# Kernel tuning notes

Hardware: AMD Instinct MI355X
Metric: run time of the kernel (lower is better)

Reference implementation:

```python
import jax, jax.numpy as jnp
import numpy as np

B, T, X, H = 8192, 2048, 1, 4

def setup_inputs() -> dict:
    key = jax.random.key(0)
    ks = jax.random.split(key, 8)
    return {
        "x": jax.random.normal(ks[0], (B, T, X), dtype=jnp.float32),
        "y": (jax.random.uniform(ks[1], (B, T)) < 0.5).astype(jnp.float32),  # binary correctness labels
        "Wxh": jax.random.normal(ks[2], (X, H), dtype=jnp.float32) * 0.5,
        "Whh": jax.random.normal(ks[3], (H, H), dtype=jnp.float32) * 0.5,
        "bh": jax.random.normal(ks[4], (H,), dtype=jnp.float32) * 0.5,
        "Wy": jax.random.normal(ks[5], (H, 4), dtype=jnp.float32) * 0.5,
        "by": jax.random.normal(ks[6], (4,), dtype=jnp.float32) * 0.5,
        "prior": jnp.float32(0.0),
    }

def _bkt_forward(x, y, Wxh, Whh, bh, Wy, by, prior):
    # x: [B,T,X], y: [B,T]. Sequential BKT scan over time with batch vectorized.
    b = x.shape[0]
    h0 = jnp.zeros((b, Wy.shape[0]), dtype=x.dtype)
    lat0 = jnp.full((b,), prior, dtype=x.dtype)

    def step(carry, xt):
        h, latent = carry
        p = jax.nn.sigmoid(h @ Wy + by)          # [B,4] -> (learn l, forget f, guess g, slip s)
        l, f, g, s = p[:, 0], p[:, 1], p[:, 2], p[:, 3]
        correct = latent * (1 - s) + (1 - latent) * g
        k_t1 = latent * (1 - s) / correct
        k_t0 = latent * s / (latent * s + (1 - latent) * (1 - g))
        m_t = k_t1 * correct + k_t0 * (1 - correct)
        new_latent = m_t * (1 - f) + (1 - m_t) * l
        h_new = jax.nn.sigmoid(xt @ Wxh + h @ Whh + bh)  # [B,H]
        return (h_new, new_latent), (correct, new_latent)

    xs = jnp.swapaxes(x, 0, 1)                   # [T,B,X]
    _, (corrects, latents) = jax.lax.scan(step, (h0, lat0), xs)
    corrects = jnp.swapaxes(corrects, 0, 1)      # [B,T]
    latents = jnp.swapaxes(latents, 0, 1)        # [B,T]
    eps = jnp.float32(1e-7)
    c = jnp.clip(corrects, eps, 1 - eps)
    loss = -jnp.mean(y * jnp.log(c) + (1 - y) * jnp.log1p(-c))
    return corrects, latents, loss

def reference(x, y, Wxh, Whh, bh, Wy, by, prior):
    return _bkt_forward(x, y, Wxh, Whh, bh, Wy, by, prior)
```

## Files before the change

### kernel.cpp

```cpp
#include <hip/hip_runtime.h>

#define BB 8192
#define TT 2048
#define CLW 16
#define WU  8

typedef __fp16 f16x2 __attribute__((ext_vector_type(2)));

__device__ __forceinline__ float sig2(float z) {
    return __builtin_amdgcn_rcpf(1.f + __builtin_amdgcn_exp2f(z));
}
__device__ __forceinline__ float sgpr(float v) {
    return __builtin_bit_cast(float, __builtin_amdgcn_readfirstlane(__builtin_bit_cast(int, v)));
}
__device__ __forceinline__ void ld16(float* d, const float* p) {
    *(float4*)(d)      = *(const float4*)(p);
    *(float4*)(d + 4)  = *(const float4*)(p + 4);
    *(float4*)(d + 8)  = *(const float4*)(p + 8);
    *(float4*)(d + 12) = *(const float4*)(p + 12);
}

__global__ __launch_bounds__(256, 4) void bkt_fused(
    const float* __restrict__ x, const float* __restrict__ y,
    const float* __restrict__ Wxh, const float* __restrict__ Whh,
    const float* __restrict__ bh, const float* __restrict__ Wy,
    const float* __restrict__ by, const float* __restrict__ prior,
    float* __restrict__ corrects, float* __restrict__ latents,
    float* __restrict__ partials)
{
    __shared__ float lds[4 * 32 * 33];
    __shared__ float2 hand[2];
    const int tid  = blockIdx.x * 256 + threadIdx.x;
    const int lane = threadIdx.x & 63;
    const int wv   = threadIdx.x >> 6;
    const int half = wv & 1;
    const int rib  = wv >> 1;
    const int row  = blockIdx.x * 2 + rib;
    float* r0 = &lds[wv * 1056];
    const int wbase = (lane >> 1) * 33 + (lane & 1) * 16;
    const float NL2E = -1.44269504088896340736f;

    const float wh00=sgpr(Whh[0]*NL2E),  wh01=sgpr(Whh[1]*NL2E),
                wh02=sgpr(Whh[2]*NL2E),  wh03=sgpr(Whh[3]*NL2E),
                wh10=sgpr(Whh[4]*NL2E),  wh11=sgpr(Whh[5]*NL2E),
                wh12=sgpr(Whh[6]*NL2E),  wh13=sgpr(Whh[7]*NL2E),
                wh20=sgpr(Whh[8]*NL2E),  wh21=sgpr(Whh[9]*NL2E),
                wh22=sgpr(Whh[10]*NL2E), wh23=sgpr(Whh[11]*NL2E),
                wh30=sgpr(Whh[12]*NL2E), wh31=sgpr(Whh[13]*NL2E),
                wh32=sgpr(Whh[14]*NL2E), wh33=sgpr(Whh[15]*NL2E);
    const float wx0=sgpr(Wxh[0]*NL2E), wx1=sgpr(Wxh[1]*NL2E),
                wx2=sgpr(Wxh[2]*NL2E), wx3=sgpr(Wxh[3]*NL2E);
    const float bh0=sgpr(bh[0]*NL2E), bh1=sgpr(bh[1]*NL2E),
                bh2=sgpr(bh[2]*NL2E), bh3=sgpr(bh[3]*NL2E);
    const float wy00=sgpr(Wy[0]*NL2E),  wy01=sgpr(Wy[1]*NL2E),
                wy02=sgpr(Wy[2]*NL2E),  wy03=sgpr(Wy[3]*NL2E),
                wy10=sgpr(Wy[4]*NL2E),  wy11=sgpr(Wy[5]*NL2E),
                wy12=sgpr(Wy[6]*NL2E),  wy13=sgpr(Wy[7]*NL2E),
                wy20=sgpr(Wy[8]*NL2E),  wy21=sgpr(Wy[9]*NL2E),
                wy22=sgpr(Wy[10]*NL2E), wy23=sgpr(Wy[11]*NL2E),
                wy30=sgpr(Wy[12]*NL2E), wy31=sgpr(Wy[13]*NL2E),
                wy32=sgpr(Wy[14]*NL2E), wy33=sgpr(Wy[15]*NL2E);
    const float by0=sgpr(by[0]*NL2E), by1=sgpr(by[1]*NL2E),
                by2=sgpr(by[2]*NL2E), by3=sgpr(by[3]*NL2E);
    const float pr = sgpr(prior[0]);

#define HSTEP(xs)                                                                   \
    {                                                                               \
        float z0 = fmaf(h3,wh30,fmaf(h2,wh20,fmaf(h1,wh10,fmaf(h0,wh00,fmaf(xs,wx0,bh0))))); \
        float z1 = fmaf(h3,wh31,fmaf(h2,wh21,fmaf(h1,wh11,fmaf(h0,wh01,fmaf(xs,wx1,bh1))))); \
        float z2 = fmaf(h3,wh32,fmaf(h2,wh22,fmaf(h1,wh12,fmaf(h0,wh02,fmaf(xs,wx2,bh2))))); \
        float z3 = fmaf(h3,wh33,fmaf(h2,wh23,fmaf(h1,wh13,fmaf(h0,wh03,fmaf(xs,wx3,bh3))))); \
        h0 = sig2(z0); h1 = sig2(z1); h2 = sig2(z2); h3 = sig2(z3);                 \
    }

    const int c  = half * 64 + lane;
    const int t0 = c * CLW;
    const float* xrow = x + (size_t)row * TT;
    float* crow = corrects + (size_t)row * TT + half * 1024;
    float* lrow = latents  + (size_t)row * TT + half * 1024;

    float xw[8], xb[16];
    {
        const float* wp = xrow + (c ? t0 - WU : 0);
        *(float4*)(xw)     = *(const float4*)(wp);
        *(float4*)(xw + 4) = *(const float4*)(wp + 4);
    }
    ld16(xb, xrow + t0);

    float h0 = 0.f, h1 = 0.f, h2 = 0.f, h3 = 0.f;
    HSTEP(xw[0])  HSTEP(xw[1])  HSTEP(xw[2])  HSTEP(xw[3])
    HSTEP(xw[4])  HSTEP(xw[5])  HSTEP(xw[6])  HSTEP(xw[7])
    if (c == 0) { h0 = h1 = h2 = h3 = 0.f; }

    float A[16], B[16];
    float Aacc = 1.f, Bacc = 0.f;
#define S1(s, DO_H)                                                                 \
    {                                                                               \
        float zl = fmaf(h3,wy30,fmaf(h2,wy20,fmaf(h1,wy10,fmaf(h0,wy00,by0))));     \
        float zf = fmaf(h3,wy31,fmaf(h2,wy21,fmaf(h1,wy11,fmaf(h0,wy01,by1))));     \
        float zg = fmaf(h3,wy32,fmaf(h2,wy22,fmaf(h1,wy12,fmaf(h0,wy02,by2))));     \
        float zs = fmaf(h3,wy33,fmaf(h2,wy23,fmaf(h1,wy13,fmaf(h0,wy03,by3))));     \
        float pl = sig2(zl), pf = sig2(zf), pgs = sig2(zg), pss = sig2(zs);         \
        float a = (1.f - pf) - pl;                                                  \
        Bacc = fmaf(a, Bacc, pl);                                                   \
        Aacc *= a;                                                                  \
        A[s] = Aacc; B[s] = Bacc;                                                   \
        f16x2 pk = __builtin_amdgcn_cvt_pkrtz(pgs, (1.f - pss) - pgs);              \
        r0[wbase + (s)] = __builtin_bit_cast(float, pk);                            \
        DO_H                                                                        \
    }
    S1(0,  HSTEP(xb[0]))  S1(1,  HSTEP(xb[1]))  S1(2,  HSTEP(xb[2]))
    S1(3,  HSTEP(xb[3]))  S1(4,  HSTEP(xb[4]))  S1(5,  HSTEP(xb[5]))
    S1(6,  HSTEP(xb[6]))  S1(7,  HSTEP(xb[7]))  S1(8,  HSTEP(xb[8]))
    S1(9,  HSTEP(xb[9]))  S1(10, HSTEP(xb[10])) S1(11, HSTEP(xb[11]))
    S1(12, HSTEP(xb[12])) S1(13, HSTEP(xb[13])) S1(14, HSTEP(xb[14]))
    S1(15, )
#undef S1

    float yb[16];
    ld16(yb, y + (size_t)row * TT + t0);

    float As = Aacc, Bs = Bacc;
#pragma unroll
    for (int off = 1; off < 64; off <<= 1) {
        float Au = __shfl_up(As, off);
        float Bu = __shfl_up(Bs, off);
        if (lane >= off) { Bs = fmaf(As, Bu, Bs); As *= Au; }
    }
    if (half == 0 && lane == 63) hand[rib] = make_float2(As, Bs);
    __syncthreads();
    float pr_base = pr;
    if (half) { const float2 hv = hand[rib]; pr_base = fmaf(hv.x, pr, hv.y); }
    const float Ae = __shfl_up(As, 1);
    const float Be = __shfl_up(Bs, 1);
    const float lat0 = (lane == 0) ? pr_base : fmaf(Ae, pr_base, Be);

    float lacc = 0.f, prod = 1.f, latp = lat0;
#define E(s)                                                                        \
    {                                                                               \
        f16x2 pk = __builtin_bit_cast(f16x2, r0[wbase + (s)]);                      \
        float cv = fmaf(latp, (float)pk[1], (float)pk[0]);                          \
        latp = fmaf(A[s], lat0, B[s]);                                              \
        float cc  = fminf(fmaxf(cv, 1e-7f), 1.f - 1e-7f);                           \
        prod *= fmaf(yb[s], fmaf(2.f, cc, -1.f), 1.f - cc);                         \
        r0[wbase + (s)] = cv;                                                       \
    }
    E(0) E(1) E(2) E(3) E(4) E(5) E(6) E(7)
    lacc += __builtin_amdgcn_logf(prod); prod = 1.f;
    E(8) E(9) E(10) E(11) E(12) E(13) E(14) E(15)
    lacc += __builtin_amdgcn_logf(prod);
#undef E

#pragma unroll
    for (int j = 0; j < 4; ++j) {
        const int base = (8 * j + (lane >> 3)) * 33 + 4 * (lane & 7);
        float4 v = make_float4(r0[base], r0[base + 1], r0[base + 2], r0[base + 3]);
        *(float4*)(crow + j * 256 + 4 * lane) = v;
    }
#pragma unroll
    for (int s = 0; s < 16; ++s) r0[wbase + s] = fmaf(A[s], lat0, B[s]);
#pragma unroll
    for (int j = 0; j < 4; ++j) {
        const int base = (8 * j + (lane >> 3)) * 33 + 4 * (lane & 7);
        float4 v = make_float4(r0[base], r0[base + 1], r0[base + 2], r0[base + 3]);
        *(float4*)(lrow + j * 256 + 4 * lane) = v;
    }

#pragma unroll
    for (int off = 32; off; off >>= 1) lacc += __shfl_down(lacc, off);
    if (lane == 0) partials[tid >> 6] = lacc;
#undef HSTEP
}

__global__ __launch_bounds__(1024) void bkt_loss(const float* __restrict__ partials, int n,
                                                 float* __restrict__ out_loss)
{
    __shared__ double sd[16];
    double s = 0.0;
    for (int i = threadIdx.x; i < n; i += 1024) s += (double)partials[i];
#pragma unroll
    for (int off = 32; off; off >>= 1) s += __shfl_down(s, off);
    if ((threadIdx.x & 63) == 0) sd[threadIdx.x >> 6] = s;
    __syncthreads();
    if (threadIdx.x == 0) {
        double t = 0.0;
#pragma unroll
        for (int k = 0; k < 16; ++k) t += sd[k];
        *out_loss = (float)(-t * 0.69314718055994530942 / ((double)BB * (double)TT));
    }
}

extern "C" void kernel_launch(void* const* d_in, const int* in_sizes, int n_in,
                              void* d_out, int out_size, void* d_ws, size_t ws_size,
                              hipStream_t stream)
{
    const float* x     = (const float*)d_in[0];
    const float* y     = (const float*)d_in[1];
    const float* Wxh   = (const float*)d_in[2];
    const float* Whh   = (const float*)d_in[3];
    const float* bh    = (const float*)d_in[4];
    const float* Wy    = (const float*)d_in[5];
    const float* by    = (const float*)d_in[6];
    const float* prior = (const float*)d_in[7];

    float* out      = (float*)d_out;
    float* corrects = out;
    float* latents  = out + (size_t)BB * TT;
    float* lossp    = out + (size_t)2 * BB * TT;

    float* partials = (float*)d_ws;

    const int nblk = BB / 2;
    bkt_fused<<<nblk, 256, 0, stream>>>(x, y, Wxh, Whh, bh, Wy, by, prior,
                                        corrects, latents, partials);
    bkt_loss<<<1, 1024, 0, stream>>>(partials, BB * 2, lossp);
}
```

Baseline: 65.89 us.

## Process a full row per wave with two interleaved chunks instead of two waves

```diff
diff --git a/kernel.cpp b/kernel.cpp
--- a/kernel.cpp
+++ b/kernel.cpp
@@ -2,7 +2,6 @@
 
 #define BB 8192
 #define TT 2048
-#define CLW 16
 #define WU  8
 
 typedef __fp16 f16x2 __attribute__((ext_vector_type(2)));
@@ -20,7 +19,7 @@
     *(float4*)(d + 12) = *(const float4*)(p + 12);
 }
 
-__global__ __launch_bounds__(256, 4) void bkt_fused(
+__global__ __launch_bounds__(256, 2) void bkt_fused(
     const float* __restrict__ x, const float* __restrict__ y,
     const float* __restrict__ Wxh, const float* __restrict__ Whh,
     const float* __restrict__ bh, const float* __restrict__ Wy,
@@ -28,16 +27,14 @@
     float* __restrict__ corrects, float* __restrict__ latents,
     float* __restrict__ partials)
 {
-    __shared__ float lds[4 * 32 * 33];
-    __shared__ float2 hand[2];
+    __shared__ float lds[4 * 64 * 33];
     const int tid  = blockIdx.x * 256 + threadIdx.x;
     const int lane = threadIdx.x & 63;
     const int wv   = threadIdx.x >> 6;
-    const int half = wv & 1;
-    const int rib  = wv >> 1;
-    const int row  = blockIdx.x * 2 + rib;
-    float* r0 = &lds[wv * 1056];
-    const int wbase = (lane >> 1) * 33 + (lane & 1) * 16;
+    const int row  = blockIdx.x * 4 + wv;
+    float* r0 = &lds[wv * 2112];
+    const int wbA = (lane >> 1) * 33 + (lane & 1) * 16;
+    const int wbB = wbA + 1056;
     const float NL2E = -1.44269504088896340736f;
 
     const float wh00=sgpr(Whh[0]*NL2E),  wh01=sgpr(Whh[1]*NL2E),
@@ -64,104 +61,148 @@
                 by2=sgpr(by[2]*NL2E), by3=sgpr(by[3]*NL2E);
     const float pr = sgpr(prior[0]);
 
-#define HSTEP(xs)                                                                   \
+#define HST(H0,H1,H2,H3,xs)                                                         \
     {                                                                               \
-        float z0 = fmaf(h3,wh30,fmaf(h2,wh20,fmaf(h1,wh10,fmaf(h0,wh00,fmaf(xs,wx0,bh0))))); \
-        float z1 = fmaf(h3,wh31,fmaf(h2,wh21,fmaf(h1,wh11,fmaf(h0,wh01,fmaf(xs,wx1,bh1))))); \
-        float z2 = fmaf(h3,wh32,fmaf(h2,wh22,fmaf(h1,wh12,fmaf(h0,wh02,fmaf(xs,wx2,bh2))))); \
-        float z3 = fmaf(h3,wh33,fmaf(h2,wh23,fmaf(h1,wh13,fmaf(h0,wh03,fmaf(xs,wx3,bh3))))); \
-        h0 = sig2(z0); h1 = sig2(z1); h2 = sig2(z2); h3 = sig2(z3);                 \
-    }
-
-    const int c  = half * 64 + lane;
-    const int t0 = c * CLW;
+        float z0 = fmaf(H3,wh30,fmaf(H2,wh20,fmaf(H1,wh10,fmaf(H0,wh00,fmaf(xs,wx0,bh0))))); \
+        float z1 = fmaf(H3,wh31,fmaf(H2,wh21,fmaf(H1,wh11,fmaf(H0,wh01,fmaf(xs,wx1,bh1))))); \
+        float z2 = fmaf(H3,wh32,fmaf(H2,wh22,fmaf(H1,wh12,fmaf(H0,wh02,fmaf(xs,wx2,bh2))))); \
+        float z3 = fmaf(H3,wh33,fmaf(H2,wh23,fmaf(H1,wh13,fmaf(H0,wh03,fmaf(xs,wx3,bh3))))); \
+        H0 = sig2(z0); H1 = sig2(z1); H2 = sig2(z2); H3 = sig2(z3);                 \
+    }
+
+    const int tA = lane * 16;
+    const int tB = 1024 + lane * 16;
     const float* xrow = x + (size_t)row * TT;
-    float* crow = corrects + (size_t)row * TT + half * 1024;
-    float* lrow = latents  + (size_t)row * TT + half * 1024;
-
-    float xw[8], xb[16];
+    const float* yrow = y + (size_t)row * TT;
+    float* crow = corrects + (size_t)row * TT;
+    float* lrow = latents  + (size_t)row * TT;
+
+    float xwA[8], xwB[8], xbA[16], xbB[16];
     {
-        const float* wp = xrow + (c ? t0 - WU : 0);
-        *(float4*)(xw)     = *(const float4*)(wp);
-        *(float4*)(xw + 4) = *(const float4*)(wp + 4);
-    }
-    ld16(xb, xrow + t0);
-
-    float h0 = 0.f, h1 = 0.f, h2 = 0.f, h3 = 0.f;
-    HSTEP(xw[0])  HSTEP(xw[1])  HSTEP(xw[2])  HSTEP(xw[3])
-    HSTEP(xw[4])  HSTEP(xw[5])  HSTEP(xw[6])  HSTEP(xw[7])
-    if (c == 0) { h0 = h1 = h2 = h3 = 0.f; }
-
-    float A[16], B[16];
-    float Aacc = 1.f, Bacc = 0.f;
-#define S1(s, DO_H)                                                                 \
+        const float* wpA = xrow + (lane ? tA - WU : 0);
+        *(float4*)(xwA)     = *(const float4*)(wpA);
+        *(float4*)(xwA + 4) = *(const float4*)(wpA + 4);
+        const float* wpB = xrow + tB - WU;
+        *(float4*)(xwB)     = *(const float4*)(wpB);
+        *(float4*)(xwB + 4) = *(const float4*)(wpB + 4);
+    }
+    ld16(xbA, xrow + tA);
+    ld16(xbB, xrow + tB);
+
+    float hA0 = 0.f, hA1 = 0.f, hA2 = 0.f, hA3 = 0.f;
+    float hB0 = 0.f, hB1 = 0.f, hB2 = 0.f, hB3 = 0.f;
+#define WUP(i) HST(hA0,hA1,hA2,hA3, xwA[i]) HST(hB0,hB1,hB2,hB3, xwB[i])
+    WUP(0) WUP(1) WUP(2) WUP(3) WUP(4) WUP(5) WUP(6) WUP(7)
+#undef WUP
+    if (lane == 0) { hA0 = hA1 = hA2 = hA3 = 0.f; }
+
+    float aplA[16], aplB[16];
+    float AckA[3], BckA[3], AckB[3], BckB[3];
+    float AaccA = 1.f, BaccA = 0.f, AaccB = 1.f, BaccB = 0.f;
+#define S1C(s, H0,H1,H2,H3, AACC,BACC, APL, WB)                                     \
     {                                                                               \
-        float zl = fmaf(h3,wy30,fmaf(h2,wy20,fmaf(h1,wy10,fmaf(h0,wy00,by0))));     \
-        float zf = fmaf(h3,wy31,fmaf(h2,wy21,fmaf(h1,wy11,fmaf(h0,wy01,by1))));     \
-        float zg = fmaf(h3,wy32,fmaf(h2,wy22,fmaf(h1,wy12,fmaf(h0,wy02,by2))));     \
-        float zs = fmaf(h3,wy33,fmaf(h2,wy23,fmaf(h1,wy13,fmaf(h0,wy03,by3))));     \
+        float zl = fmaf(H3,wy30,fmaf(H2,wy20,fmaf(H1,wy10,fmaf(H0,wy00,by0))));     \
+        float zf = fmaf(H3,wy31,fmaf(H2,wy21,fmaf(H1,wy11,fmaf(H0,wy01,by1))));     \
+        float zg = fmaf(H3,wy32,fmaf(H2,wy22,fmaf(H1,wy12,fmaf(H0,wy02,by2))));     \
+        float zs = fmaf(H3,wy33,fmaf(H2,wy23,fmaf(H1,wy13,fmaf(H0,wy03,by3))));     \
         float pl = sig2(zl), pf = sig2(zf), pgs = sig2(zg), pss = sig2(zs);         \
         float a = (1.f - pf) - pl;                                                  \
-        Bacc = fmaf(a, Bacc, pl);                                                   \
-        Aacc *= a;                                                                  \
-        A[s] = Aacc; B[s] = Bacc;                                                   \
-        f16x2 pk = __builtin_amdgcn_cvt_pkrtz(pgs, (1.f - pss) - pgs);              \
-        r0[wbase + (s)] = __builtin_bit_cast(float, pk);                            \
-        DO_H                                                                        \
-    }
-    S1(0,  HSTEP(xb[0]))  S1(1,  HSTEP(xb[1]))  S1(2,  HSTEP(xb[2]))
-    S1(3,  HSTEP(xb[3]))  S1(4,  HSTEP(xb[4]))  S1(5,  HSTEP(xb[5]))
-    S1(6,  HSTEP(xb[6]))  S1(7,  HSTEP(xb[7]))  S1(8,  HSTEP(xb[8]))
-    S1(9,  HSTEP(xb[9]))  S1(10, HSTEP(xb[10])) S1(11, HSTEP(xb[11]))
-    S1(12, HSTEP(xb[12])) S1(13, HSTEP(xb[13])) S1(14, HSTEP(xb[14]))
-    S1(15, )
-#undef S1
-
-    float yb[16];
-    ld16(yb, y + (size_t)row * TT + t0);
-
-    float As = Aacc, Bs = Bacc;
+        BACC = fmaf(a, BACC, pl);                                                   \
+        AACC *= a;                                                                  \
+        f16x2 pk0 = __builtin_amdgcn_cvt_pkrtz(pgs, (1.f - pss) - pgs);             \
+        f16x2 pk1 = __builtin_amdgcn_cvt_pkrtz(a, pl);                              \
+        r0[(WB) + (s)] = __builtin_bit_cast(float, pk0);                            \
+        APL[s] = __builtin_bit_cast(float, pk1);                                    \
+    }
+#define STEP2(s)                                                                    \
+    S1C(s, hA0,hA1,hA2,hA3, AaccA,BaccA, aplA, wbA)                                 \
+    S1C(s, hB0,hB1,hB2,hB3, AaccB,BaccB, aplB, wbB)                                 \
+    HST(hA0,hA1,hA2,hA3, xbA[s]) HST(hB0,hB1,hB2,hB3, xbB[s])
+#define CKP(k) AckA[k]=AaccA; BckA[k]=BaccA; AckB[k]=AaccB; BckB[k]=BaccB;
+    STEP2(0)  STEP2(1)  STEP2(2)  STEP2(3)  CKP(0)
+    STEP2(4)  STEP2(5)  STEP2(6)  STEP2(7)  CKP(1)
+    STEP2(8)  STEP2(9)  STEP2(10) STEP2(11) CKP(2)
+    STEP2(12) STEP2(13) STEP2(14)
+    S1C(15, hA0,hA1,hA2,hA3, AaccA,BaccA, aplA, wbA)
+    S1C(15, hB0,hB1,hB2,hB3, AaccB,BaccB, aplB, wbB)
+#undef CKP
+#undef STEP2
+#undef S1C
+
+    float AsA = AaccA, BsA = BaccA, AsB = AaccB, BsB = BaccB;
 #pragma unroll
     for (int off = 1; off < 64; off <<= 1) {
-        float Au = __shfl_up(As, off);
-        float Bu = __shfl_up(Bs, off);
-        if (lane >= off) { Bs = fmaf(As, Bu, Bs); As *= Au; }
-    }
-    if (half == 0 && lane == 63) hand[rib] = make_float2(As, Bs);
-    __syncthreads();
-    float pr_base = pr;
-    if (half) { const float2 hv = hand[rib]; pr_base = fmaf(hv.x, pr, hv.y); }
-    const float Ae = __shfl_up(As, 1);
-    const float Be = __shfl_up(Bs, 1);
-    const float lat0 = (lane == 0) ? pr_base : fmaf(Ae, pr_base, Be);
-
-    float lacc = 0.f, prod = 1.f, latp = lat0;
-#define E(s)                                                                        \
+        float Au = __shfl_up(AsA, off), Bu = __shfl_up(BsA, off);
+        float Cu = __shfl_up(AsB, off), Du = __shfl_up(BsB, off);
+        if (lane >= off) {
+            BsA = fmaf(AsA, Bu, BsA); AsA *= Au;
+            BsB = fmaf(AsB, Du, BsB); AsB *= Cu;
+        }
+    }
+    const float AeA = __shfl_up(AsA, 1), BeA = __shfl_up(BsA, 1);
+    const float latA0 = (lane == 0) ? pr : fmaf(AeA, pr, BeA);
+    const float Am = __shfl(AsA, 63), Bm = __shfl(BsA, 63);
+    const float prB = fmaf(Am, pr, Bm);
+    const float AeB = __shfl_up(AsB, 1), BeB = __shfl_up(BsB, 1);
+    const float latB0 = (lane == 0) ? prB : fmaf(AeB, prB, BeB);
+
+    float ybA[16], ybB[16];
+    ld16(ybA, yrow + tA);
+    ld16(ybB, yrow + tB);
+    float lacc = 0.f, prodA = 1.f, prodB = 1.f;
+    float latpA = latA0, latpB = latB0;
+#define EC(s, LATP, APL, WB, Y, PROD)                                               \
     {                                                                               \
-        f16x2 pk = __builtin_bit_cast(f16x2, r0[wbase + (s)]);                      \
-        float cv = fmaf(latp, (float)pk[1], (float)pk[0]);                          \
-        latp = fmaf(A[s], lat0, B[s]);                                              \
+        f16x2 pk0 = __builtin_bit_cast(f16x2, r0[(WB) + (s)]);                      \
+        f16x2 pk1 = __builtin_bit_cast(f16x2, APL[s]);                              \
+        float cv = fmaf(LATP, (float)pk0[1], (float)pk0[0]);                        \
+        LATP = fmaf((float)pk1[0], LATP, (float)pk1[1]);                            \
         float cc  = fminf(fmaxf(cv, 1e-7f), 1.f - 1e-7f);                           \
-        prod *= fmaf(yb[s], fmaf(2.f, cc, -1.f), 1.f - cc);                         \
-        r0[wbase + (s)] = cv;                                                       \
-    }
-    E(0) E(1) E(2) E(3) E(4) E(5) E(6) E(7)
-    lacc += __builtin_amdgcn_logf(prod); prod = 1.f;
-    E(8) E(9) E(10) E(11) E(12) E(13) E(14) E(15)
-    lacc += __builtin_amdgcn_logf(prod);
-#undef E
-
-#pragma unroll
-    for (int j = 0; j < 4; ++j) {
-        const int base = (8 * j + (lane >> 3)) * 33 + 4 * (lane & 7);
+        PROD *= fmaf(Y[s], fmaf(2.f, cc, -1.f), 1.f - cc);                          \
+        r0[(WB) + (s)] = cv;                                                        \
+    }
+#define E2(s) EC(s, latpA, aplA, wbA, ybA, prodA) EC(s, latpB, aplB, wbB, ybB, prodB)
+#define RST(k) latpA = fmaf(AckA[k], latA0, BckA[k]); latpB = fmaf(AckB[k], latB0, BckB[k]);
+    E2(0)  E2(1)  E2(2)  E2(3)  RST(0)
+    E2(4)  E2(5)  E2(6)  E2(7)  RST(1)
+    lacc += __builtin_amdgcn_logf(prodA) + __builtin_amdgcn_logf(prodB);
+    prodA = 1.f; prodB = 1.f;
+    E2(8)  E2(9)  E2(10) E2(11) RST(2)
+    E2(12) E2(13) E2(14) E2(15)
+    lacc += __builtin_amdgcn_logf(prodA) + __builtin_amdgcn_logf(prodB);
+#undef E2
+#undef EC
+
+    const int rr = lane >> 2;
+#pragma unroll
+    for (int j = 0; j < 8; ++j) {
+        const int base = (8 * j + (rr >> 1)) * 33 + (rr & 1) * 16 + 4 * (lane & 3);
         float4 v = make_float4(r0[base], r0[base + 1], r0[base + 2], r0[base + 3]);
         *(float4*)(crow + j * 256 + 4 * lane) = v;
     }
-#pragma unroll
-    for (int s = 0; s < 16; ++s) r0[wbase + s] = fmaf(A[s], lat0, B[s]);
-#pragma unroll
-    for (int j = 0; j < 4; ++j) {
-        const int base = (8 * j + (lane >> 3)) * 33 + 4 * (lane & 7);
+    {
+        float lqA = latA0, lqB = latB0;
+#define L2(s)                                                                       \
+        {                                                                           \
+            f16x2 pA = __builtin_bit_cast(f16x2, aplA[s]);                          \
+            f16x2 pB = __builtin_bit_cast(f16x2, aplB[s]);                          \
+            lqA = fmaf((float)pA[0], lqA, (float)pA[1]);                            \
+            lqB = fmaf((float)pB[0], lqB, (float)pB[1]);                            \
+            r0[wbA + (s)] = lqA;                                                    \
+            r0[wbB + (s)] = lqB;                                                    \
+        }
+        L2(0)  L2(1)  L2(2)  L2(3)
+        lqA = fmaf(AckA[0], latA0, BckA[0]); lqB = fmaf(AckB[0], latB0, BckB[0]);
+        L2(4)  L2(5)  L2(6)  L2(7)
+        lqA = fmaf(AckA[1], latA0, BckA[1]); lqB = fmaf(AckB[1], latB0, BckB[1]);
+        L2(8)  L2(9)  L2(10) L2(11)
+        lqA = fmaf(AckA[2], latA0, BckA[2]); lqB = fmaf(AckB[2], latB0, BckB[2]);
+        L2(12) L2(13) L2(14) L2(15)
+#undef L2
+    }
+#pragma unroll
+    for (int j = 0; j < 8; ++j) {
+        const int base = (8 * j + (rr >> 1)) * 33 + (rr & 1) * 16 + 4 * (lane & 3);
         float4 v = make_float4(r0[base], r0[base + 1], r0[base + 2], r0[base + 3]);
         *(float4*)(lrow + j * 256 + 4 * lane) = v;
     }
@@ -169,7 +210,8 @@
 #pragma unroll
     for (int off = 32; off; off >>= 1) lacc += __shfl_down(lacc, off);
     if (lane == 0) partials[tid >> 6] = lacc;
-#undef HSTEP
+#undef HST
+#undef RST
 }
 
 __global__ __launch_bounds__(1024) void bkt_loss(const float* __restrict__ partials, int n,
@@ -210,8 +252,8 @@
 
     float* partials = (float*)d_ws;
 
-    const int nblk = BB / 2;
+    const int nblk = BB / 4;
     bkt_fused<<<nblk, 256, 0, stream>>>(x, y, Wxh, Whh, bh, Wy, by, prior,
                                         corrects, latents, partials);
-    bkt_loss<<<1, 1024, 0, stream>>>(partials, BB * 2, lossp);
-}
+    bkt_loss<<<1, 1024, 0, stream>>>(partials, BB, lossp);
+}
```

Measured after the change: 64.95 us. About the same (-1.4%).
